# Optimization experiments

Hardware: AMD Instinct MI355X
Metric: run time of the kernel (lower is better)

The kernel has to match this reference:

```python
import jax, jax.numpy as jnp
import numpy as np

B, N, H, W = 8, 500000, 512, 512
HALF_CENTOR = True
BIG = jnp.float32(3.4e38)  # sentinel for invalid points in segment_min


def setup_inputs() -> dict:
    key = jax.random.key(0)
    k1, k2 = jax.random.split(key)
    # continuous (x, y) coords in grid units; slightly out of bounds to exercise the mask
    points = jax.random.uniform(k1, (B, N, 2), minval=-8.0, maxval=520.0, dtype=jnp.float32)
    costs = jax.random.normal(k2, (B, N), dtype=jnp.float32)
    default_cost = jnp.zeros([], jnp.float32)  # trainable scalar (default_type='DYNAMIC')
    return {"points": points, "costs": costs, "default_cost": default_cost,
            "height": H, "width": W}


def reference(points, costs, default_cost, height, width):
    b, n, _ = points.shape
    half = 0.5 if HALF_CENTOR else 0.0
    ix = jnp.floor(points[..., 0] + half).astype(jnp.int32)  # [B, N]
    iy = jnp.floor(points[..., 1] + half).astype(jnp.int32)
    valid = (ix >= 0) & (ix < width) & (iy >= 0) & (iy < height)
    bidx = jnp.broadcast_to(jnp.arange(b, dtype=jnp.int32)[:, None], (b, n))
    nseg = b * height * width
    # invalid points routed to an extra trash segment that is sliced off
    seg = jnp.where(valid, (bidx * height + iy) * width + ix, nseg).reshape(-1)
    cmin = jax.ops.segment_min(jnp.where(valid, costs, BIG).reshape(-1), seg,
                               num_segments=nseg + 1)[:nseg]
    count = jax.ops.segment_sum(valid.reshape(-1).astype(jnp.int32), seg,
                                num_segments=nseg + 1)[:nseg]
    cost_mask = (count - 1).reshape(b, height, width)  # -1 where cell empty (MIN semantics)
    cost = jnp.where(cost_mask >= 0, cmin.reshape(b, height, width), default_cost)
    return cost, cost_mask
```

## Files before the change

kernel.cpp:

```cpp
#include <hip/hip_runtime.h>


#define CHUNK 8192
#define TPB 512
#define NIT 8
constexpr int HH = 512, WW = 512;
constexpr int NBINS = 512;
constexpr int CAP = 16384;

__device__ __forceinline__ unsigned f2ord(float f) {
    unsigned u = __float_as_uint(f);
    return (u & 0x80000000u) ? ~u : (u | 0x80000000u);
}
__device__ __forceinline__ float ord2f(unsigned u) {
    return __uint_as_float((u & 0x80000000u) ? (u & 0x7FFFFFFFu) : ~u);
}

__global__ void pInit(unsigned* __restrict__ gcur) {
    gcur[threadIdx.x] = (unsigned)(threadIdx.x * CAP);
}

__global__ __launch_bounds__(TPB) void pS(const float4* __restrict__ pts4,
                                          const float2* __restrict__ cst2,
                                          unsigned* __restrict__ gcur,
                                          unsigned* __restrict__ sorted,
                                          int npts, int N) {
    __shared__ unsigned hist[NBINS];
    __shared__ unsigned gbase[NBINS];
    const int t = threadIdx.x, blk = blockIdx.x;
    hist[t] = 0u;
    __syncthreads();

    const int base = blk * CHUNK;
    const int vbase = base >> 1;
    const int b0 = base / N;
    const int boundary = (b0 + 1) * N;

    unsigned rec[2 * NIT];
    unsigned pack[2 * NIT];

    int g = vbase + t;
    bool in0 = (base + 2 * t) < npts;
    float4 P = in0 ? pts4[g] : make_float4(-100.f, -100.f, -100.f, -100.f);
    float2 C = in0 ? cst2[g] : make_float2(0.f, 0.f);
#pragma unroll
    for (int k = 0; k < NIT; ++k) {
        float4 Pc = P;
        float2 Cc = C;
        const int idx0 = base + 2 * (k * TPB + t);
        if (k + 1 < NIT) {
            int gn = vbase + (k + 1) * TPB + t;
            bool in = (base + 2 * ((k + 1) * TPB + t)) < npts;
            P = in ? pts4[gn] : make_float4(-100.f, -100.f, -100.f, -100.f);
            C = in ? cst2[gn] : make_float2(0.f, 0.f);
        }
#pragma unroll
        for (int j = 0; j < 2; ++j) {
            const int idx = idx0 + j;
            const float px = j ? Pc.z : Pc.x;
            const float py = j ? Pc.w : Pc.y;
            const float cv = j ? Cc.y : Cc.x;
            int ix = (int)floorf(px + 0.5f);
            int iy = (int)floorf(py + 0.5f);
            unsigned pk = 0xFFFFFFFFu, rc = 0u;
            if (ix >= 0 && ix < WW && iy >= 0 && iy < HH) {
                int b = (idx >= boundary) ? b0 + 1 : b0;
                unsigned bin = (unsigned)(b * 64 + ((iy >> 6) << 3) + (ix >> 6));
                unsigned lc  = (unsigned)(((iy & 63) << 6) | (ix & 63));
                unsigned rank = atomicAdd(&hist[bin], 1u);
                pk = (bin << 13) | rank;
                rc = (lc << 20) | (f2ord(cv) >> 12);
            }
            rec[2 * k + j]  = rc;
            pack[2 * k + j] = pk;
        }
    }
    __syncthreads();

    gbase[t] = atomicAdd(&gcur[t], hist[t]);
    __syncthreads();

#pragma unroll
    for (int k = 0; k < 2 * NIT; ++k) {
        if (pack[k] != 0xFFFFFFFFu) {
            unsigned bin = pack[k] >> 13, rank = pack[k] & 8191u;
            unsigned slot = gbase[bin] + rank;
            if (slot < (bin + 1u) * CAP)
                sorted[slot] = rec[k];
        }
    }
}

__global__ __launch_bounds__(TPB) void pD(const unsigned* __restrict__ sorted,
                                          const unsigned* __restrict__ gcur,
                                          const float* __restrict__ def,
                                          float* __restrict__ out_cost,
                                          float* __restrict__ out_mask) {
    __shared__ unsigned mn[4096];
    __shared__ unsigned ct[4096];
    const int bin = blockIdx.x, t = threadIdx.x;
#pragma unroll
    for (int i = t; i < 4096; i += TPB) { mn[i] = 0xFFFFFFFFu; ct[i] = 0u; }
    __syncthreads();
    const unsigned s0 = (unsigned)bin * CAP;
    const unsigned e  = gcur[bin];
    const unsigned s1 = (e < s0 + CAP) ? e : s0 + CAP;
    for (unsigned i = s0 + t; i < s1; i += TPB) {
        unsigned v = sorted[i];
        atomicMin(&mn[v >> 20], v & 0xFFFFFu);
        atomicAdd(&ct[v >> 20], 1u);
    }
    __syncthreads();
    const float d = *def;
    const int b = bin >> 6, tile = bin & 63, ty = tile >> 3, tx = tile & 7;
    const int r = t >> 3, c0 = (t & 7) * 8;
    const int o0 = (b * HH + ty * 64 + r) * WW + tx * 64 + c0;
#pragma unroll
    for (int v4 = 0; v4 < 2; ++v4) {
        float4 oc, om;
        float* pc = (float*)&oc;
        float* pm = (float*)&om;
#pragma unroll
        for (int j = 0; j < 4; ++j) {
            int i = r * 64 + c0 + v4 * 4 + j;
            unsigned cc = ct[i];
            pc[j] = cc ? ord2f((mn[i] << 12) | 0x800u) : d;
            pm[j] = (float)((int)cc - 1);
        }
        *(float4*)(out_cost + o0 + v4 * 4) = oc;
        *(float4*)(out_mask + o0 + v4 * 4) = om;
    }
}

__global__ void fb_init(uint2* __restrict__ cells, int nseg) {
    int i = blockIdx.x * blockDim.x + threadIdx.x;
    int stride = gridDim.x * blockDim.x;
    for (; i < nseg; i += stride) cells[i] = make_uint2(0xFFFFFFFFu, 0u);
}
__global__ void fb_scatter(const float2* __restrict__ pts, const float* __restrict__ costs,
                           uint2* __restrict__ cells, int npts, int N, int H, int W) {
    int i = blockIdx.x * blockDim.x + threadIdx.x;
    if (i >= npts) return;
    float2 p = pts[i];
    int ix = (int)floorf(p.x + 0.5f), iy = (int)floorf(p.y + 0.5f);
    if (ix < 0 || ix >= W || iy < 0 || iy >= H) return;
    int b = i / N;
    atomicMin(&cells[(b * H + iy) * W + ix].x, f2ord(costs[i]));
    atomicAdd(&cells[(b * H + iy) * W + ix].y, 1u);
}
__global__ void fb_final(const uint2* __restrict__ cells, const float* __restrict__ def,
                         float* __restrict__ oc, float* __restrict__ om, int nseg) {
    int i = blockIdx.x * blockDim.x + threadIdx.x;
    if (i >= nseg) return;
    uint2 c = cells[i];
    float d = *def;
    oc[i] = c.y ? ord2f(c.x) : d;
    om[i] = (float)((int)c.y - 1);
}

extern "C" void kernel_launch(void* const* d_in, const int* in_sizes, int n_in,
                              void* d_out, int out_size, void* d_ws, size_t ws_size,
                              hipStream_t stream) {
    const float2* pts = (const float2*)d_in[0];
    const float*  cst = (const float*)d_in[1];
    const float*  def = (const float*)d_in[2];

    const int npts = in_sizes[1];
    const int nseg = out_size / 2;
    const int B    = nseg / (HH * WW);
    const int N    = npts / B;
    float* out_cost = (float*)d_out;
    float* out_mask = out_cost + nseg;

    const int NB = (npts + CHUNK - 1) / CHUNK;
    const size_t sorted_bytes = (size_t)NBINS * CAP * 4;
    const size_t need = sorted_bytes + NBINS * 4;
    const bool cap_ok = (npts / NBINS) * 2 <= CAP;

    if (B == 8 && nseg == 8 * HH * WW && ws_size >= need && N > CHUNK &&
        cap_ok && (npts % 2) == 0) {
        unsigned* sorted = (unsigned*)d_ws;
        unsigned* gcur   = (unsigned*)((char*)d_ws + sorted_bytes);

        pInit<<<1,     TPB, 0, stream>>>(gcur);
        pS   <<<NB,    TPB, 0, stream>>>((const float4*)pts, (const float2*)cst,
                                         gcur, sorted, npts, N);
        pD   <<<NBINS, TPB, 0, stream>>>(sorted, gcur, def, out_cost, out_mask);
    } else {
        uint2* cells = (uint2*)d_ws;
        fb_init   <<<2048, 256, 0, stream>>>(cells, nseg);
        fb_scatter<<<(npts + 255) / 256, 256, 0, stream>>>(pts, cst, cells, npts, N, HH, WW);
        fb_final  <<<(nseg + 255) / 256, 256, 0, stream>>>(cells, def, out_cost, out_mask, nseg);
    }
}
```

Before: 118.9 us.

## Stage bucketed records in LDS for coalesced global writes; vectorize bin reads

The scatter kernel now computes a block-local exclusive prefix over bin histograms, places records into a shared-memory staging buffer in bin order, and then has each wavefront copy whole bin runs to global memory contiguously. This replaces scattered single-word global stores with coalesced runs. Global atomics are skipped for empty bins. The reduce kernel reads sorted records as uint4 vectors with a scalar tail. Costs include 32KB of extra LDS per block, which may lower occupancy, plus extra barriers.

```diff
diff --git a/kernel.cpp b/kernel.cpp
--- a/kernel.cpp
+++ b/kernel.cpp
@@ -27,6 +27,9 @@
                                           int npts, int N) {
     __shared__ unsigned hist[NBINS];
     __shared__ unsigned gbase[NBINS];
+    __shared__ unsigned lbase[NBINS];
+    __shared__ unsigned wsum[TPB / 64];
+    __shared__ unsigned srec[CHUNK];
     const int t = threadIdx.x, blk = blockIdx.x;
     hist[t] = 0u;
     __syncthreads();
@@ -77,16 +80,54 @@
     }
     __syncthreads();
 
-    gbase[t] = atomicAdd(&gcur[t], hist[t]);
+    {
+        const unsigned v = hist[t];
+        unsigned gb = 0u;
+        if (v) gb = atomicAdd(&gcur[t], v);
+        unsigned s = v;
+#pragma unroll
+        for (int d = 1; d < 64; d <<= 1) {
+            unsigned n = __shfl_up(s, d);
+            if ((t & 63) >= d) s += n;
+        }
+        if ((t & 63) == 63) wsum[t >> 6] = s;
+        gbase[t] = gb;
+        __syncthreads();
+        if (t == 0) {
+            unsigned acc = 0;
+#pragma unroll
+            for (int i = 0; i < TPB / 64; ++i) { unsigned x = wsum[i]; wsum[i] = acc; acc += x; }
+        }
+        __syncthreads();
+        lbase[t] = wsum[t >> 6] + s - v;
+    }
     __syncthreads();
 
 #pragma unroll
     for (int k = 0; k < 2 * NIT; ++k) {
         if (pack[k] != 0xFFFFFFFFu) {
             unsigned bin = pack[k] >> 13, rank = pack[k] & 8191u;
-            unsigned slot = gbase[bin] + rank;
-            if (slot < (bin + 1u) * CAP)
-                sorted[slot] = rec[k];
+            srec[lbase[bin] + rank] = rec[k];
+        }
+    }
+    __syncthreads();
+
+    {
+        const int w = t >> 6, lane = t & 63;
+        const int lastIdx = (base + CHUNK < npts ? base + CHUNK : npts) - 1;
+        const int b1 = lastIdx / N;
+        const int bmin = b0 * 64;
+        const int bmax = (b1 + 1) * 64;
+        for (int bin = bmin + w; bin < bmax; bin += TPB / 64) {
+            unsigned len = hist[bin];
+            if (!len) continue;
+            const unsigned lb = lbase[bin];
+            const unsigned gb = gbase[bin];
+            const unsigned cap = (unsigned)(bin + 1) * CAP;
+            const unsigned maxn = (gb < cap) ? (cap - gb) : 0u;
+            if (len > maxn) len = maxn;
+            for (unsigned off = (unsigned)lane; off < len; off += 64u)
+                sorted[gb + off] = srec[lb + off];
         }
     }
 }
@@ -105,8 +146,18 @@
     const unsigned s0 = (unsigned)bin * CAP;
     const unsigned e  = gcur[bin];
     const unsigned s1 = (e < s0 + CAP) ? e : s0 + CAP;
-    for (unsigned i = s0 + t; i < s1; i += TPB) {
-        unsigned v = sorted[i];
+    const unsigned len = s1 - s0;
+    const unsigned nv = len >> 2;
+    const uint4* sp = (const uint4*)(sorted + s0);
+    for (unsigned i = (unsigned)t; i < nv; i += TPB) {
+        uint4 v = sp[i];
+        atomicMin(&mn[v.x >> 20], v.x & 0xFFFFFu); atomicAdd(&ct[v.x >> 20], 1u);
+        atomicMin(&mn[v.y >> 20], v.y & 0xFFFFFu); atomicAdd(&ct[v.y >> 20], 1u);
+        atomicMin(&mn[v.z >> 20], v.z & 0xFFFFFu); atomicAdd(&ct[v.z >> 20], 1u);
+        atomicMin(&mn[v.w >> 20], v.w & 0xFFFFFu); atomicAdd(&ct[v.w >> 20], 1u);
+    }
+    for (unsigned i = (nv << 2) + (unsigned)t; i < len; i += TPB) {
+        unsigned v = sorted[s0 + i];
         atomicMin(&mn[v >> 20], v & 0xFFFFFu);
         atomicAdd(&ct[v >> 20], 1u);
     }
```

Measured after the change: 109.9 us. 1.08x faster.
